# Performance work log

Measured on AMD Instinct MI355X. Metric: run time of the kernel, lower is better.

Reference implementation:

```python
import jax, jax.numpy as jnp
import numpy as np

N, D, H, C = 100000, 128, 8, 16  # nodes, units=H*C, heads, per-head channels
E = 400000                        # edges per edge set (2 edge sets)
LN_EPS = 1e-3                     # keras LayerNormalization default epsilon


def setup_inputs() -> dict:
    key = jax.random.key(0)
    ks = jax.random.split(key, 16)
    def dense(k, i, o):
        return jax.random.normal(k, (i, o), jnp.float32) / np.float32(np.sqrt(i))
    return dict(
        x=jax.random.normal(ks[0], (N, D), jnp.float32),
        src0=jax.random.randint(ks[1], (E,), 0, N),
        dst0=jax.random.randint(ks[2], (E,), 0, N),
        src1=jax.random.randint(ks[3], (E,), 0, N),
        dst1=jax.random.randint(ks[4], (E,), 0, N),
        Wk=dense(ks[5], D, D), bk=jnp.zeros((D,), jnp.float32),
        Wm=dense(ks[6], D, D), bm=jnp.zeros((D,), jnp.float32),
        Wq=dense(ks[7], D, D), bq=jnp.zeros((D,), jnp.float32),
        Wa=dense(ks[8], D, D), ba=jnp.zeros((D,), jnp.float32),
        Watt0=jax.random.normal(ks[9], (H, C, C), jnp.float32) / np.float32(np.sqrt(C)),
        Wmsg0=jax.random.normal(ks[10], (H, C, C), jnp.float32) / np.float32(np.sqrt(C)),
        Watt1=jax.random.normal(ks[11], (H, C, C), jnp.float32) / np.float32(np.sqrt(C)),
        Wmsg1=jax.random.normal(ks[12], (H, C, C), jnp.float32) / np.float32(np.sqrt(C)),
        prior0=jnp.ones((H,), jnp.float32),
        prior1=jnp.ones((H,), jnp.float32),
        skip=jnp.ones((), jnp.float32),
        gamma=jnp.ones((D,), jnp.float32),
        beta=jnp.zeros((D,), jnp.float32),
    )


def reference(x, src0, dst0, src1, dst1, Wk, bk, Wm, bm, Wq, bq, Wa, ba,
              Watt0, Wmsg0, Watt1, Wmsg1, prior0, prior1, skip, gamma, beta):
    # Node-level projections, split per head: [N, H, C]
    k = (x @ Wk + bk).reshape(N, H, C)
    m = (x @ Wm + bm).reshape(N, H, C)
    q = (x @ Wq + bq).reshape(N, H, C)
    scale = 1.0 / jnp.sqrt(jnp.float32(C))

    def edge_terms(src, dst, Watt, Wmsg, prior):
        # per-edge-type relation projections of gathered sender keys/messages
        ke = jnp.einsum('ehk,hkl->ehl', k[src], Watt)          # [E, H, C]
        score = jnp.einsum('ehl,ehl->eh', ke, q[dst]) * prior * scale  # [E, H]
        msg = jnp.einsum('ehk,hkl->ehl', m[src], Wmsg)          # [E, H, C]
        return score, msg

    s0, m0 = edge_terms(src0, dst0, Watt0, Wmsg0, prior0)
    s1, m1 = edge_terms(src1, dst1, Watt1, Wmsg1, prior1)

    # Joint segment softmax over all incoming edges (both edge sets) per receiver
    scores = jnp.concatenate([s0, s1], axis=0)   # [2E, H]
    msgs = jnp.concatenate([m0, m1], axis=0)     # [2E, H, C]
    recv = jnp.concatenate([dst0, dst1], axis=0)

    smax = jax.ops.segment_max(scores, recv, num_segments=N)   # [N, H]
    ex = jnp.exp(scores - smax[recv])
    denom = jax.ops.segment_sum(ex, recv, num_segments=N)      # [N, H]
    d_e = denom[recv]
    attn = ex / jnp.where(d_e > 0, d_e, 1.0)                   # [2E, H]

    pooled = jax.ops.segment_sum(attn[:, :, None] * msgs, recv,
                                 num_segments=N).reshape(N, D)  # [N, D]

    # aggr(gelu(pooled)); weighted skip; layer norm
    h = jax.nn.gelu(pooled, approximate=False) @ Wa + ba
    alpha = jax.nn.sigmoid(skip)
    out = alpha * h + (1.0 - alpha) * x
    mu = jnp.mean(out, axis=-1, keepdims=True)
    var = jnp.var(out, axis=-1, keepdims=True)
    out = (out - mu) * jax.lax.rsqrt(var + LN_EPS) * gamma + beta
    return out
```

## Files before the change

kernel.cpp:

```cpp
#include <hip/hip_runtime.h>
#include <hip/hip_bf16.h>
#include <math.h>

#define N_NODES 100000
#define DIM 128
#define NH 8
#define NC 16
#define E_EDGES 400000
#define LN_EPS 1e-3f
#define SCAN_B 1024
#define PROJ_GRID 512

typedef __attribute__((ext_vector_type(8))) short short8v;
typedef __attribute__((ext_vector_type(4))) short short4v;
typedef __attribute__((ext_vector_type(4))) float float4v;

__device__ __forceinline__ short bf16bits(float v) {
    __hip_bfloat16 b = __float2bfloat16(v);
    return *(short*)&b;
}

__global__ __launch_bounds__(128) void fuse_weights(
    const float* __restrict__ Wk, const float* __restrict__ bk,
    const float* __restrict__ Wm, const float* __restrict__ bm,
    const float* __restrict__ Wq, const float* __restrict__ bq,
    const float* __restrict__ Wa, const float* __restrict__ ba,
    const float* __restrict__ Watt0, const float* __restrict__ Wmsg0,
    const float* __restrict__ Watt1, const float* __restrict__ Wmsg1,
    const float* __restrict__ prior0, const float* __restrict__ prior1,
    __hip_bfloat16* __restrict__ Wt, float* __restrict__ bias)
{
    const int c = blockIdx.x;
    const int d = threadIdx.x;
    const int sec = c >> 7, j = c & 127, h = j >> 4, l = j & 15;
    float v, b;
    if (sec == 4)      { v = Wq[d * DIM + j]; b = bq[j]; }
    else if (sec == 5) { v = Wa[d * DIM + j]; b = ba[j]; }
    else {
        const float* W1 = (sec < 2) ? Wk : Wm;
        const float* bs = (sec < 2) ? bk : bm;
        const float* W2 = (sec == 0) ? Watt0 : (sec == 1) ? Watt1
                          : (sec == 2) ? Wmsg0 : Wmsg1;
        float scale = (sec == 0) ? prior0[h] * 0.25f
                    : (sec == 1) ? prior1[h] * 0.25f : 1.f;
        float s = 0.f, sb = 0.f;
        #pragma unroll
        for (int kk = 0; kk < NC; ++kk) {
            float w2 = W2[h * 256 + kk * 16 + l];
            s  = fmaf(W1[d * DIM + h * 16 + kk], w2, s);
            sb = fmaf(bs[h * 16 + kk], w2, sb);
        }
        v = s * scale; b = sb * scale;
    }
    Wt[(size_t)c * DIM + d] = __float2bfloat16(v);
    if (d == 0) bias[c] = b;
}

__global__ __launch_bounds__(512) void proj_mfma(
    const float* __restrict__ x,
    const __hip_bfloat16* __restrict__ Wt,
    const float* __restrict__ bias,
    __hip_bfloat16* __restrict__ kattC,
    __hip_bfloat16* __restrict__ mmsgC,
    __hip_bfloat16* __restrict__ qb)
{
    __shared__ __align__(16) short xs[2][32 * DIM];
    const int tid = threadIdx.x;
    const int wave = tid >> 6, lane = tid & 63;
    const int quad = lane >> 4, mcol = lane & 15;
    const int nt = N_NODES / 32;

    short8v wf[5][4];
    float4v bv[5];
    #pragma unroll
    for (int s = 0; s < 5; ++s) {
        const int c0 = s * 128 + wave * 16;
        const short* wp = (const short*)Wt + (size_t)(c0 + mcol) * DIM + quad * 8;
        #pragma unroll
        for (int kb = 0; kb < 4; ++kb)
            wf[s][kb] = *(const short8v*)(wp + kb * 32);
        bv[s] = *(const float4v*)(bias + c0 + quad * 4);
    }

    const int srow = tid >> 4, sc8 = tid & 15;
    const int swz = ((sc8 ^ (srow & 7)) * 8);

    int t = blockIdx.x;
    if (t >= nt) return;

    float4v f0 = *(const float4v*)(x + (size_t)(t * 32 + srow) * DIM + sc8 * 8);
    float4v f1 = *(const float4v*)(x + (size_t)(t * 32 + srow) * DIM + sc8 * 8 + 4);
    {
        short8v sv;
        #pragma unroll
        for (int j = 0; j < 4; ++j) { sv[j] = bf16bits(f0[j]); sv[j + 4] = bf16bits(f1[j]); }
        *(short8v*)(xs[0] + srow * DIM + swz) = sv;
    }
    {
        int nn = t + PROJ_GRID;
        if (nn < nt) {
            f0 = *(const float4v*)(x + (size_t)(nn * 32 + srow) * DIM + sc8 * 8);
            f1 = *(const float4v*)(x + (size_t)(nn * 32 + srow) * DIM + sc8 * 8 + 4);
        }
    }

    int cur = 0;
    for (; t < nt; t += PROJ_GRID) {
        __syncthreads();

        short8v b0[4], b1[4];
        #pragma unroll
        for (int kb = 0; kb < 4; ++kb) {
            const int ch = ((quad + kb * 4) ^ (mcol & 7)) * 8;
            b0[kb] = *(const short8v*)(xs[cur] + mcol * DIM + ch);
            b1[kb] = *(const short8v*)(xs[cur] + (mcol + 16) * DIM + ch);
        }

        const int r0 = t * 32;
        #pragma unroll
        for (int s = 0; s < 5; ++s) {
            float4v acc0 = {0.f, 0.f, 0.f, 0.f};
            float4v acc1 = {0.f, 0.f, 0.f, 0.f};
            #pragma unroll
            for (int kb = 0; kb < 4; ++kb) {
                acc0 = __builtin_amdgcn_mfma_f32_16x16x32_bf16(wf[s][kb], b0[kb], acc0, 0, 0, 0);
                acc1 = __builtin_amdgcn_mfma_f32_16x16x32_bf16(wf[s][kb], b1[kb], acc1, 0, 0, 0);
            }
            __hip_bfloat16* dst =
                (s == 0) ? kattC :
                (s == 1) ? kattC + (size_t)N_NODES * DIM :
                (s == 2) ? mmsgC :
                (s == 3) ? mmsgC + (size_t)N_NODES * DIM :
                           qb;
            short* drow0 = (short*)dst + (size_t)(r0 + mcol) * DIM + wave * 16 + quad * 4;
            short4v o0, o1;
            #pragma unroll
            for (int g = 0; g < 4; ++g) {
                o0[g] = bf16bits(acc0[g] + bv[s][g]);
                o1[g] = bf16bits(acc1[g] + bv[s][g]);
            }
            *(short4v*)drow0              = o0;
            *(short4v*)(drow0 + 16 * DIM) = o1;
        }

        int nn = t + PROJ_GRID;
        if (nn < nt) {
            short8v sv;
            #pragma unroll
            for (int j = 0; j < 4; ++j) { sv[j] = bf16bits(f0[j]); sv[j + 4] = bf16bits(f1[j]); }
            *(short8v*)(xs[cur ^ 1] + srow * DIM + swz) = sv;
            int n2 = nn + PROJ_GRID;
            if (n2 < nt) {
                f0 = *(const float4v*)(x + (size_t)(n2 * 32 + srow) * DIM + sc8 * 8);
                f1 = *(const float4v*)(x + (size_t)(n2 * 32 + srow) * DIM + sc8 * 8 + 4);
            }
        }
        cur ^= 1;
    }
}

__global__ __launch_bounds__(256) void hist_kernel(
    const int* __restrict__ dst0, const int* __restrict__ dst1,
    int* __restrict__ counts)
{
    int e = blockIdx.x * 256 + threadIdx.x;
    if (e < E_EDGES) atomicAdd(&counts[dst0[e]], 1);
    int e1 = e - E_EDGES;
    if (e1 >= 0 && e1 < E_EDGES) atomicAdd(&counts[dst1[e1]], 1);
}

__global__ __launch_bounds__(SCAN_B) void scanA_kernel(
    const int* __restrict__ counts, int* __restrict__ row_ptr,
    int* __restrict__ bsum)
{
    __shared__ int buf[2][SCAN_B];
    int i = blockIdx.x * SCAN_B + threadIdx.x;
    int v = (i < N_NODES) ? counts[i] : 0;
    int cur = 0;
    buf[0][threadIdx.x] = v;
    __syncthreads();
    #pragma unroll
    for (int off = 1; off < SCAN_B; off <<= 1) {
        int t = buf[cur][threadIdx.x];
        int add = (threadIdx.x >= off) ? buf[cur][threadIdx.x - off] : 0;
        buf[cur ^ 1][threadIdx.x] = t + add;
        cur ^= 1;
        __syncthreads();
    }
    int inc = buf[cur][threadIdx.x];
    if (i < N_NODES) row_ptr[i] = inc - v;
    if (threadIdx.x == SCAN_B - 1) bsum[blockIdx.x] = inc;
}

__global__ __launch_bounds__(128) void scanB_kernel(int* __restrict__ bsum, int nblocks)
{
    __shared__ int buf[2][128];
    int t = threadIdx.x;
    int v = (t < nblocks) ? bsum[t] : 0;
    buf[0][t] = v;
    __syncthreads();
    int cur = 0;
    #pragma unroll
    for (int off = 1; off < 128; off <<= 1) {
        int a = buf[cur][t];
        if (t >= off) a += buf[cur][t - off];
        buf[cur ^ 1][t] = a;
        cur ^= 1;
        __syncthreads();
    }
    if (t < nblocks) bsum[t] = buf[cur][t] - v;
}

__global__ __launch_bounds__(SCAN_B) void scanC_kernel(
    int* __restrict__ row_ptr, int* __restrict__ cursor,
    const int* __restrict__ bsum)
{
    int i = blockIdx.x * SCAN_B + threadIdx.x;
    if (i < N_NODES) {
        int r = row_ptr[i] + bsum[blockIdx.x];
        row_ptr[i] = r;
        cursor[i] = r;
    }
}

__global__ __launch_bounds__(256) void scatter_kernel(
    const int* __restrict__ src0, const int* __restrict__ dst0,
    const int* __restrict__ src1, const int* __restrict__ dst1,
    int* __restrict__ cursor, unsigned int* __restrict__ eidx)
{
    int e = blockIdx.x * 256 + threadIdx.x;
    if (e < E_EDGES) {
        int d = dst0[e];
        int pos = atomicAdd(&cursor[d], 1);
        eidx[pos] = (unsigned int)src0[e];
    }
    int e1 = e - E_EDGES;
    if (e1 >= 0 && e1 < E_EDGES) {
        int d = dst1[e1];
        int pos = atomicAdd(&cursor[d], 1);
        eidx[pos] = (unsigned int)(src1[e1] + N_NODES);
    }
}

__global__ __launch_bounds__(256) void agg_kernel(
    const __hip_bfloat162* __restrict__ katt,
    const __hip_bfloat162* __restrict__ mmsg,
    const __hip_bfloat162* __restrict__ qb2,
    const int* __restrict__ row_ptr, const int* __restrict__ counts,
    const unsigned int* __restrict__ eidx,
    __hip_bfloat162* __restrict__ pooled2)
{
    const int wave = threadIdx.x >> 6, lane = threadIdx.x & 63;
    const int n = blockIdx.x * 4 + wave;
    if (n >= N_NODES) return;
    const int start = row_ptr[n], cnt = counts[n];
    __hip_bfloat162 qv = qb2[(size_t)n * 64 + lane];
    const float qx = __bfloat162float(qv.x), qy = __bfloat162float(qv.y);

    float accx = 0.f, accy = 0.f, den = 0.f;
    int i = 0;
    for (; i + 2 <= cnt; i += 2) {
        unsigned int r0 = eidx[start + i];
        unsigned int r1 = eidx[start + i + 1];
        __hip_bfloat162 ka0 = katt[(size_t)r0 * 64 + lane];
        __hip_bfloat162 ka1 = katt[(size_t)r1 * 64 + lane];
        __hip_bfloat162 mg0 = mmsg[(size_t)r0 * 64 + lane];
        __hip_bfloat162 mg1 = mmsg[(size_t)r1 * 64 + lane];
        float p0 = fmaf(__bfloat162float(ka0.x), qx,
                        __bfloat162float(ka0.y) * qy);
        float p1 = fmaf(__bfloat162float(ka1.x), qx,
                        __bfloat162float(ka1.y) * qy);
        p0 += __shfl_xor(p0, 1, 64); p0 += __shfl_xor(p0, 2, 64); p0 += __shfl_xor(p0, 4, 64);
        p1 += __shfl_xor(p1, 1, 64); p1 += __shfl_xor(p1, 2, 64); p1 += __shfl_xor(p1, 4, 64);
        float e0 = __expf(p0), e1 = __expf(p1);
        accx = fmaf(e0, __bfloat162float(mg0.x), accx);
        accy = fmaf(e0, __bfloat162float(mg0.y), accy);
        accx = fmaf(e1, __bfloat162float(mg1.x), accx);
        accy = fmaf(e1, __bfloat162float(mg1.y), accy);
        den += e0 + e1;
    }
    if (i < cnt) {
        unsigned int r0 = eidx[start + i];
        __hip_bfloat162 ka0 = katt[(size_t)r0 * 64 + lane];
        __hip_bfloat162 mg0 = mmsg[(size_t)r0 * 64 + lane];
        float p0 = fmaf(__bfloat162float(ka0.x), qx,
                        __bfloat162float(ka0.y) * qy);
        p0 += __shfl_xor(p0, 1, 64); p0 += __shfl_xor(p0, 2, 64); p0 += __shfl_xor(p0, 4, 64);
        float e0 = __expf(p0);
        accx = fmaf(e0, __bfloat162float(mg0.x), accx);
        accy = fmaf(e0, __bfloat162float(mg0.y), accy);
        den += e0;
    }

    float vx = 0.f, vy = 0.f;
    if (den > 0.f) { vx = accx / den; vy = accy / den; }
    vx = 0.5f * vx * (1.f + erff(vx * 0.70710678118654752f));
    vy = 0.5f * vy * (1.f + erff(vy * 0.70710678118654752f));
    __hip_bfloat162 o; o.x = __float2bfloat16(vx); o.y = __float2bfloat16(vy);
    pooled2[(size_t)n * 64 + lane] = o;
}

__global__ __launch_bounds__(256) void final_mfma(
    const __hip_bfloat16* __restrict__ pooled,
    const __hip_bfloat16* __restrict__ Wt,
    const float* __restrict__ bias,
    const float* __restrict__ x,
    const float* __restrict__ skip, const float* __restrict__ gamma,
    const float* __restrict__ beta, float* __restrict__ out)
{
    __shared__ float hs[32][DIM];
    const int wave = threadIdx.x >> 6, lane = threadIdx.x & 63;
    const int quad = lane >> 4, mcol = lane & 15;
    const int r0 = blockIdx.x * 32;

    short8v a0[4], a1[4];
    const short* pp0 = (const short*)pooled + (size_t)(r0 + mcol) * DIM + quad * 8;
    const short* pp1 = pp0 + 16 * DIM;
    #pragma unroll
    for (int kb = 0; kb < 4; ++kb) {
        a0[kb] = *(const short8v*)(pp0 + kb * 32);
        a1[kb] = *(const short8v*)(pp1 + kb * 32);
    }
    const float alpha = 1.f / (1.f + expf(-skip[0]));

    #pragma unroll
    for (int t = 0; t < 2; ++t) {
        const int c0 = wave * 32 + t * 16;
        const short* wp = (const short*)Wt + (size_t)(640 + c0 + mcol) * DIM + quad * 8;
        float4v acc0 = {0.f, 0.f, 0.f, 0.f};
        float4v acc1 = {0.f, 0.f, 0.f, 0.f};
        #pragma unroll
        for (int kb = 0; kb < 4; ++kb) {
            short8v bfr = *(const short8v*)(wp + kb * 32);
            acc0 = __builtin_amdgcn_mfma_f32_16x16x32_bf16(a0[kb], bfr, acc0, 0, 0, 0);
            acc1 = __builtin_amdgcn_mfma_f32_16x16x32_bf16(a1[kb], bfr, acc1, 0, 0, 0);
        }
        const float bcol = bias[640 + c0 + mcol];
        const int cc = c0 + mcol;
        const int rq = quad * 4;
        #pragma unroll
        for (int g = 0; g < 4; ++g) {
            int rA = rq + g, rB = rq + 16 + g;
            hs[rA][cc] = alpha * (acc0[g] + bcol)
                       + (1.f - alpha) * x[(size_t)(r0 + rA) * DIM + cc];
            hs[rB][cc] = alpha * (acc1[g] + bcol)
                       + (1.f - alpha) * x[(size_t)(r0 + rB) * DIM + cc];
        }
    }
    __syncthreads();

    float gam0 = gamma[lane], gam1 = gamma[lane + 64];
    float bet0 = beta[lane],  bet1 = beta[lane + 64];
    for (int r = wave; r < 32; r += 4) {
        int row = r0 + r;
        float v0 = hs[r][lane], v1 = hs[r][lane + 64];
        float s = v0 + v1, s2 = v0 * v0 + v1 * v1;
        #pragma unroll
        for (int off = 1; off < 64; off <<= 1) {
            s  += __shfl_xor(s,  off, 64);
            s2 += __shfl_xor(s2, off, 64);
        }
        float mu = s * (1.f / 128.f);
        float var = s2 * (1.f / 128.f) - mu * mu;
        float rstd = rsqrtf(var + LN_EPS);
        out[(size_t)row * DIM + lane]      = (v0 - mu) * rstd * gam0 + bet0;
        out[(size_t)row * DIM + lane + 64] = (v1 - mu) * rstd * gam1 + bet1;
    }
}

extern "C" void kernel_launch(void* const* d_in, const int* in_sizes, int n_in,
                              void* d_out, int out_size, void* d_ws, size_t ws_size,
                              hipStream_t stream) {
    const float* x     = (const float*)d_in[0];
    const int*   src0  = (const int*)d_in[1];
    const int*   dst0  = (const int*)d_in[2];
    const int*   src1  = (const int*)d_in[3];
    const int*   dst1  = (const int*)d_in[4];
    const float* Wk    = (const float*)d_in[5];
    const float* bk    = (const float*)d_in[6];
    const float* Wm    = (const float*)d_in[7];
    const float* bm    = (const float*)d_in[8];
    const float* Wq    = (const float*)d_in[9];
    const float* bq    = (const float*)d_in[10];
    const float* Wa    = (const float*)d_in[11];
    const float* ba    = (const float*)d_in[12];
    const float* Watt0 = (const float*)d_in[13];
    const float* Wmsg0 = (const float*)d_in[14];
    const float* Watt1 = (const float*)d_in[15];
    const float* Wmsg1 = (const float*)d_in[16];
    const float* prior0= (const float*)d_in[17];
    const float* prior1= (const float*)d_in[18];
    const float* skip  = (const float*)d_in[19];
    const float* gamma = (const float*)d_in[20];
    const float* beta  = (const float*)d_in[21];
    float* out = (float*)d_out;

    const size_t nd = (size_t)N_NODES * DIM;
    char* wsb = (char*)d_ws;
    __hip_bfloat16* Wt    = (__hip_bfloat16*)wsb;  wsb += (size_t)768 * DIM * 2;
    float* bias           = (float*)wsb;           wsb += 768 * 4;
    __hip_bfloat16* kattC = (__hip_bfloat16*)wsb;  wsb += 2 * nd * 2;
    __hip_bfloat16* mmsgC = (__hip_bfloat16*)wsb;  wsb += 2 * nd * 2;
    __hip_bfloat16* qb    = (__hip_bfloat16*)wsb;  wsb += nd * 2;
    __hip_bfloat16* pooled= (__hip_bfloat16*)wsb;  wsb += nd * 2;
    int* counts  = (int*)wsb;                      wsb += (size_t)N_NODES * 4;
    int* row_ptr = (int*)wsb;                      wsb += (size_t)N_NODES * 4;
    int* cursor  = (int*)wsb;                      wsb += (size_t)N_NODES * 4;
    int* bsum    = (int*)wsb;                      wsb += 128 * 4;
    unsigned int* eidx = (unsigned int*)wsb;

    hipMemsetAsync(counts, 0, (size_t)N_NODES * 4, stream);

    const int scan_blocks = (N_NODES + SCAN_B - 1) / SCAN_B;
    const int edge_blocks = (2 * E_EDGES + 255) / 256;

    hist_kernel<<<dim3(edge_blocks), dim3(256), 0, stream>>>(dst0, dst1, counts);
    scanA_kernel<<<dim3(scan_blocks), dim3(SCAN_B), 0, stream>>>(counts, row_ptr, bsum);
    scanB_kernel<<<dim3(1), dim3(128), 0, stream>>>(bsum, scan_blocks);
    scanC_kernel<<<dim3(scan_blocks), dim3(SCAN_B), 0, stream>>>(row_ptr, cursor, bsum);
    scatter_kernel<<<dim3(edge_blocks), dim3(256), 0, stream>>>(
        src0, dst0, src1, dst1, cursor, eidx);

    fuse_weights<<<dim3(768), dim3(128), 0, stream>>>(
        Wk, bk, Wm, bm, Wq, bq, Wa, ba,
        Watt0, Wmsg0, Watt1, Wmsg1, prior0, prior1, Wt, bias);
    proj_mfma<<<dim3(PROJ_GRID), dim3(512), 0, stream>>>(
        x, Wt, bias, kattC, mmsgC, qb);

    agg_kernel<<<dim3((N_NODES + 3) / 4), dim3(256), 0, stream>>>(
        (const __hip_bfloat162*)kattC, (const __hip_bfloat162*)mmsgC,
        (const __hip_bfloat162*)qb, row_ptr, counts, eidx,
        (__hip_bfloat162*)pooled);

    final_mfma<<<dim3(N_NODES / 32), dim3(256), 0, stream>>>(
        pooled, Wt, bias, x, skip, gamma, beta, out);
}
```

Baseline: 372.9 us.

## Interleave key and message rows so each edge gathers one contiguous 512-byte row

The projection kernel now writes the relation-projected keys and messages for each (edge type, source node) into one 256-wide bf16 row, keys in the first half and messages in the second. The aggregation kernel fetches that row with a single 8-byte load per lane. Lanes 0-31 compute scores and lanes 32-63 accumulate messages, with the exp weight passed across halves by shuffle. The edge loop is unrolled by four to keep more gathers in flight, and bf16 is unpacked with bit shifts. The aim is to halve the number of separate gather transactions and raise memory-level parallelism, at the cost of some lanes doing redundant score math.

```diff
diff --git a/kernel.cpp b/kernel.cpp
--- a/kernel.cpp
+++ b/kernel.cpp
@@ -18,6 +18,11 @@
 __device__ __forceinline__ short bf16bits(float v) {
     __hip_bfloat16 b = __float2bfloat16(v);
     return *(short*)&b;
+}
+
+__device__ __forceinline__ void bf2x2(unsigned v, float& a, float& b) {
+    a = __uint_as_float(v << 16);
+    b = __uint_as_float(v & 0xffff0000u);
 }
 
 __global__ __launch_bounds__(128) void fuse_weights(
@@ -60,8 +65,7 @@
     const float* __restrict__ x,
     const __hip_bfloat16* __restrict__ Wt,
     const float* __restrict__ bias,
-    __hip_bfloat16* __restrict__ kattC,
-    __hip_bfloat16* __restrict__ mmsgC,
+    __hip_bfloat16* __restrict__ km,
     __hip_bfloat16* __restrict__ qb)
 {
     __shared__ __align__(16) short xs[2][32 * DIM];
@@ -126,21 +130,24 @@
                 acc0 = __builtin_amdgcn_mfma_f32_16x16x32_bf16(wf[s][kb], b0[kb], acc0, 0, 0, 0);
                 acc1 = __builtin_amdgcn_mfma_f32_16x16x32_bf16(wf[s][kb], b1[kb], acc1, 0, 0, 0);
             }
-            __hip_bfloat16* dst =
-                (s == 0) ? kattC :
-                (s == 1) ? kattC + (size_t)N_NODES * DIM :
-                (s == 2) ? mmsgC :
-                (s == 3) ? mmsgC + (size_t)N_NODES * DIM :
-                           qb;
-            short* drow0 = (short*)dst + (size_t)(r0 + mcol) * DIM + wave * 16 + quad * 4;
             short4v o0, o1;
             #pragma unroll
             for (int g = 0; g < 4; ++g) {
                 o0[g] = bf16bits(acc0[g] + bv[s][g]);
                 o1[g] = bf16bits(acc1[g] + bv[s][g]);
             }
-            *(short4v*)drow0              = o0;
-            *(short4v*)(drow0 + 16 * DIM) = o1;
+            if (s < 4) {
+                size_t row = (size_t)(r0 + mcol) + ((s & 1) ? (size_t)N_NODES : 0);
+                short* dp = (short*)km + row * 256 + ((s & 2) ? 128 : 0)
+                          + wave * 16 + quad * 4;
+                *(short4v*)dp              = o0;
+                *(short4v*)(dp + 16 * 256) = o1;
+            } else {
+                short* dp = (short*)qb + (size_t)(r0 + mcol) * DIM
+                          + wave * 16 + quad * 4;
+                *(short4v*)dp              = o0;
+                *(short4v*)(dp + 16 * DIM) = o1;
+            }
         }
 
         int nn = t + PROJ_GRID;
@@ -243,61 +250,75 @@
 }
 
 __global__ __launch_bounds__(256) void agg_kernel(
-    const __hip_bfloat162* __restrict__ katt,
-    const __hip_bfloat162* __restrict__ mmsg,
-    const __hip_bfloat162* __restrict__ qb2,
+    const uint2* __restrict__ km,
+    const uint2* __restrict__ qv,
     const int* __restrict__ row_ptr, const int* __restrict__ counts,
     const unsigned int* __restrict__ eidx,
-    __hip_bfloat162* __restrict__ pooled2)
+    unsigned int* __restrict__ pooled)
 {
     const int wave = threadIdx.x >> 6, lane = threadIdx.x & 63;
     const int n = blockIdx.x * 4 + wave;
     if (n >= N_NODES) return;
     const int start = row_ptr[n], cnt = counts[n];
-    __hip_bfloat162 qv = qb2[(size_t)n * 64 + lane];
-    const float qx = __bfloat162float(qv.x), qy = __bfloat162float(qv.y);
-
-    float accx = 0.f, accy = 0.f, den = 0.f;
+    const int low = lane & 31;
+
+    uint2 qu = qv[(size_t)n * 32 + low];
+    float q0, q1, q2, q3;
+    bf2x2(qu.x, q0, q1); bf2x2(qu.y, q2, q3);
+
+    float a0 = 0.f, a1 = 0.f, a2 = 0.f, a3 = 0.f, den = 0.f;
+
+#define EDGE_ACC(u)                                                          \
+    {                                                                        \
+        float c0, c1, c2, c3;                                                \
+        bf2x2((u).x, c0, c1); bf2x2((u).y, c2, c3);                          \
+        float p = fmaf(c3, q3, fmaf(c2, q2, fmaf(c1, q1, c0 * q0)));         \
+        p += __shfl_xor(p, 1, 64); p += __shfl_xor(p, 2, 64);                \
+        float e = __expf(p);                                                 \
+        den += e;                                                            \
+        float eb = __shfl_xor(e, 32, 64);                                    \
+        a0 = fmaf(eb, c0, a0); a1 = fmaf(eb, c1, a1);                        \
+        a2 = fmaf(eb, c2, a2); a3 = fmaf(eb, c3, a3);                        \
+    }
+
     int i = 0;
-    for (; i + 2 <= cnt; i += 2) {
-        unsigned int r0 = eidx[start + i];
-        unsigned int r1 = eidx[start + i + 1];
-        __hip_bfloat162 ka0 = katt[(size_t)r0 * 64 + lane];
-        __hip_bfloat162 ka1 = katt[(size_t)r1 * 64 + lane];
-        __hip_bfloat162 mg0 = mmsg[(size_t)r0 * 64 + lane];
-        __hip_bfloat162 mg1 = mmsg[(size_t)r1 * 64 + lane];
-        float p0 = fmaf(__bfloat162float(ka0.x), qx,
-                        __bfloat162float(ka0.y) * qy);
-        float p1 = fmaf(__bfloat162float(ka1.x), qx,
-                        __bfloat162float(ka1.y) * qy);
-        p0 += __shfl_xor(p0, 1, 64); p0 += __shfl_xor(p0, 2, 64); p0 += __shfl_xor(p0, 4, 64);
-        p1 += __shfl_xor(p1, 1, 64); p1 += __shfl_xor(p1, 2, 64); p1 += __shfl_xor(p1, 4, 64);
-        float e0 = __expf(p0), e1 = __expf(p1);
-        accx = fmaf(e0, __bfloat162float(mg0.x), accx);
-        accy = fmaf(e0, __bfloat162float(mg0.y), accy);
-        accx = fmaf(e1, __bfloat162float(mg1.x), accx);
-        accy = fmaf(e1, __bfloat162float(mg1.y), accy);
-        den += e0 + e1;
-    }
-    if (i < cnt) {
-        unsigned int r0 = eidx[start + i];
-        __hip_bfloat162 ka0 = katt[(size_t)r0 * 64 + lane];
-        __hip_bfloat162 mg0 = mmsg[(size_t)r0 * 64 + lane];
-        float p0 = fmaf(__bfloat162float(ka0.x), qx,
-                        __bfloat162float(ka0.y) * qy);
-        p0 += __shfl_xor(p0, 1, 64); p0 += __shfl_xor(p0, 2, 64); p0 += __shfl_xor(p0, 4, 64);
-        float e0 = __expf(p0);
-        accx = fmaf(e0, __bfloat162float(mg0.x), accx);
-        accy = fmaf(e0, __bfloat162float(mg0.y), accy);
-        den += e0;
-    }
-
-    float vx = 0.f, vy = 0.f;
-    if (den > 0.f) { vx = accx / den; vy = accy / den; }
-    vx = 0.5f * vx * (1.f + erff(vx * 0.70710678118654752f));
-    vy = 0.5f * vy * (1.f + erff(vy * 0.70710678118654752f));
-    __hip_bfloat162 o; o.x = __float2bfloat16(vx); o.y = __float2bfloat16(vy);
-    pooled2[(size_t)n * 64 + lane] = o;
+    for (; i + 4 <= cnt; i += 4) {
+        unsigned r0i = eidx[start + i];
+        unsigned r1i = eidx[start + i + 1];
+        unsigned r2i = eidx[start + i + 2];
+        unsigned r3i = eidx[start + i + 3];
+        uint2 u0 = km[(size_t)r0i * 64 + lane];
+        uint2 u1 = km[(size_t)r1i * 64 + lane];
+        uint2 u2 = km[(size_t)r2i * 64 + lane];
+        uint2 u3 = km[(size_t)r3i * 64 + lane];
+        EDGE_ACC(u0); EDGE_ACC(u1); EDGE_ACC(u2); EDGE_ACC(u3);
+    }
+    for (; i < cnt; ++i) {
+        unsigned r0i = eidx[start + i];
+        uint2 u0 = km[(size_t)r0i * 64 + lane];
+        EDGE_ACC(u0);
+    }
+#undef EDGE_ACC
+
+    float denb = __shfl_xor(den, 32, 64);
+    float v0 = 0.f, v1 = 0.f, v2 = 0.f, v3 = 0.f;
+    if (denb > 0.f) {
+        float inv = 1.f / denb;
+        v0 = a0 * inv; v1 = a1 * inv; v2 = a2 * inv; v3 = a3 * inv;
+    }
+    v0 = 0.5f * v0 * (1.f + erff(v0 * 0.70710678118654752f));
+    v1 = 0.5f * v1 * (1.f + erff(v1 * 0.70710678118654752f));
+    v2 = 0.5f * v2 * (1.f + erff(v2 * 0.70710678118654752f));
+    v3 = 0.5f * v3 * (1.f + erff(v3 * 0.70710678118654752f));
+
+    if (lane >= 32) {
+        unsigned plo = ((unsigned)(unsigned short)bf16bits(v0))
+                     | ((unsigned)(unsigned short)bf16bits(v1) << 16);
+        unsigned phi = ((unsigned)(unsigned short)bf16bits(v2))
+                     | ((unsigned)(unsigned short)bf16bits(v3) << 16);
+        pooled[(size_t)n * 64 + (lane - 32) * 2]     = plo;
+        pooled[(size_t)n * 64 + (lane - 32) * 2 + 1] = phi;
+    }
 }
 
 __global__ __launch_bounds__(256) void final_mfma(
@@ -399,8 +420,7 @@
     char* wsb = (char*)d_ws;
     __hip_bfloat16* Wt    = (__hip_bfloat16*)wsb;  wsb += (size_t)768 * DIM * 2;
     float* bias           = (float*)wsb;           wsb += 768 * 4;
-    __hip_bfloat16* kattC = (__hip_bfloat16*)wsb;  wsb += 2 * nd * 2;
-    __hip_bfloat16* mmsgC = (__hip_bfloat16*)wsb;  wsb += 2 * nd * 2;
+    __hip_bfloat16* km    = (__hip_bfloat16*)wsb;  wsb += (size_t)2 * N_NODES * 256 * 2;
     __hip_bfloat16* qb    = (__hip_bfloat16*)wsb;  wsb += nd * 2;
     __hip_bfloat16* pooled= (__hip_bfloat16*)wsb;  wsb += nd * 2;
     int* counts  = (int*)wsb;                      wsb += (size_t)N_NODES * 4;
@@ -425,12 +445,11 @@
         Wk, bk, Wm, bm, Wq, bq, Wa, ba,
         Watt0, Wmsg0, Watt1, Wmsg1, prior0, prior1, Wt, bias);
     proj_mfma<<<dim3(PROJ_GRID), dim3(512), 0, stream>>>(
-        x, Wt, bias, kattC, mmsgC, qb);
+        x, Wt, bias, km, qb);
 
     agg_kernel<<<dim3((N_NODES + 3) / 4), dim3(256), 0, stream>>>(
-        (const __hip_bfloat162*)kattC, (const __hip_bfloat162*)mmsgC,
-        (const __hip_bfloat162*)qb, row_ptr, counts, eidx,
-        (__hip_bfloat162*)pooled);
+        (const uint2*)km, (const uint2*)qb, row_ptr, counts, eidx,
+        (unsigned int*)pooled);
 
     final_mfma<<<dim3(N_NODES / 32), dim3(256), 0, stream>>>(
         pooled, Wt, bias, x, skip, gamma, beta, out);
```

Result: no change. 370.5 us (-0.6%).
